# Performance work log

Measured on AMD Instinct MI355X. Metric: run time of the kernel, lower is better.

The kernel has to match this reference:

```python
import jax, jax.numpy as jnp
import numpy as np
import math

B, L, C_IN = 64, 3168, 64
D_MODEL, K = 512, 16  # K = cycle_length (kernel width == stride)
W = L // K            # 198 output tokens from deform conv


def _positional(S, d, dtype):
    # PositionalEmbedding buffer, rows [0, S)
    pos = jnp.arange(S, dtype=jnp.float32)[:, None]
    div = jnp.exp(jnp.arange(0, d, 2, dtype=jnp.float32) * (-math.log(10000.0) / d))
    pe = jnp.zeros((S, d), jnp.float32)
    pe = pe.at[:, 0::2].set(jnp.sin(pos * div))
    pe = pe.at[:, 1::2].set(jnp.cos(pos * div))
    return pe.astype(dtype)


def setup_inputs() -> dict:
    key = jax.random.key(0)
    ks = jax.random.split(key, 6)
    fan_in = C_IN * K
    std = math.sqrt(2.0 / (1 + 0.01 ** 2) / fan_in)  # kaiming_normal, leaky_relu fan_in
    return {
        "x": jax.random.normal(ks[0], (B, L, C_IN), jnp.float32),
        "w_off": jax.random.normal(ks[1], (2 * K, C_IN, K), jnp.float32) * std,
        "b_off": jax.random.normal(ks[2], (2 * K,), jnp.float32) * 0.02,
        "w_def": jax.random.normal(ks[3], (D_MODEL, C_IN, K), jnp.float32) * std,
        "b_def": jax.random.normal(ks[4], (D_MODEL,), jnp.float32) * 0.02,
        "cls_token": jax.random.normal(ks[5], (1, 1, D_MODEL), jnp.float32),
    }


def _gather_cols(xt, idx, L_):
    # xt: (B, C, L); idx: (B, K, W) int32 -> (B, C, K, W), zero out-of-bounds
    b, c = xt.shape[0], xt.shape[1]
    valid = (idx >= 0) & (idx < L_)
    idxc = jnp.clip(idx, 0, L_ - 1).reshape(b, 1, -1)
    g = jnp.take_along_axis(xt, jnp.broadcast_to(idxc, (b, c, idxc.shape[-1])), axis=2)
    g = g.reshape(b, c, idx.shape[1], idx.shape[2])
    return jnp.where(valid[:, None], g, 0.0)


def reference(x, w_off, b_off, w_def, b_def, cls_token):
    b, l, c = x.shape
    w = l // K
    # offset conv: kernel (1,K), stride (1,K) == non-overlapping windows
    xr = x[:, : w * K, :].reshape(b, w, K, c)              # (B, W, K, C)
    off = jnp.einsum('bwkc,ock->bow', xr, w_off) + b_off[None, :, None]  # (B, 2K, W)
    dy = off[:, 0::2]                                      # (B, K, W)
    dx = off[:, 1::2]
    # sampling positions along width (height is size 1, base y = 0)
    base = (jnp.arange(w)[None, :] * K + jnp.arange(K)[:, None]).astype(x.dtype)  # (K, W)
    px = base[None] + dx                                   # (B, K, W)
    x0 = jnp.floor(px)
    frac = px - x0
    x0i = x0.astype(jnp.int32)
    xt = x.transpose(0, 2, 1)                              # (B, C, L)
    v0 = _gather_cols(xt, x0i, l)
    v1 = _gather_cols(xt, x0i + 1, l)
    wy = jnp.maximum(0.0, 1.0 - jnp.abs(dy))               # vertical bilinear weight on row 0
    val = wy[:, None] * ((1.0 - frac)[:, None] * v0 + frac[:, None] * v1)  # (B, C, K, W)
    out = jnp.einsum('bckw,dck->bwd', val, w_def) + b_def  # (B, W, d_model)
    tok = jnp.concatenate([jnp.broadcast_to(cls_token, (b, 1, D_MODEL)), out], axis=1)
    pe = _positional(w + 1, D_MODEL, tok.dtype)
    return tok + pe[None]
```

## Files before the change

kernel.cpp:

```cpp
#include <hip/hip_runtime.h>
#include <math.h>
#include <stdint.h>

#define NB 64
#define NL 3168
#define NC 64
#define ND 512
#define NK 16
#define NW 198
#define NM 12672
#define KD 1024

typedef __attribute__((ext_vector_type(8))) short bf8_t;
typedef __attribute__((ext_vector_type(4))) float f4_t;

typedef const unsigned int __attribute__((address_space(1)))* as1_u32p;
typedef unsigned int __attribute__((address_space(3)))* as3_u32p;

__device__ __forceinline__ void gl_lds16(const void* g, void* l) {
  __builtin_amdgcn_global_load_lds((as1_u32p)(uintptr_t)g,
                                   (as3_u32p)(unsigned int)(uintptr_t)l, 16, 0, 0);
}

__device__ __forceinline__ unsigned short f2bf(float f) {
  union { float f; unsigned u; } v; v.f = f;
  unsigned r = v.u + 0x7FFFu + ((v.u >> 16) & 1u);
  return (unsigned short)(r >> 16);
}

__global__ void prep_kernel(const float* __restrict__ w_off, const float* __restrict__ w_def,
                            const float* __restrict__ cls, unsigned short* __restrict__ wofft,
                            unsigned short* __restrict__ wdeft, float* __restrict__ pe,
                            float* __restrict__ out) {
  int id = blockIdx.x * 256 + threadIdx.x;
  if (id < 131072) {
    float4 v = ((const float4*)w_def)[id];
    ushort4 o;
    o.x = f2bf(v.x); o.y = f2bf(v.y); o.z = f2bf(v.z); o.w = f2bf(v.w);
    ((ushort4*)wdeft)[id] = o;
    return;
  }
  id -= 131072;
  if (id < 32768) {
    int o = id >> 10, kc = id & 1023, k = kc >> 6, c = kc & 63;
    wofft[id] = f2bf(w_off[o * 1024 + c * 16 + k]);
    return;
  }
  id -= 32768;
  if (id < 101888) {
    int pos = id >> 9, d = id & 511;
    int i = d >> 1;
    float freq = expf((float)(2 * i) * (-9.210340371976184f / 512.0f));
    float arg = (float)pos * freq;
    pe[id] = (d & 1) ? cosf(arg) : sinf(arg);
    return;
  }
  id -= 101888;
  {
    int b = id >> 9, d = id & 511;
    out[(size_t)(b * 199) * 512 + d] = cls[d] + ((d & 1) ? 1.0f : 0.0f);
  }
}

__launch_bounds__(512)
__global__ void offsample_kernel(const float* __restrict__ x,
                                 const unsigned short* __restrict__ wofft,
                                 const float* __restrict__ b_off,
                                 unsigned short* __restrict__ val_ws) {
  __shared__ float partial[8][16][33];
  __shared__ float offs[16][32];
  int tid = threadIdx.x;
  int lane = tid & 63, wid = tid >> 6;
  int r16 = lane & 15, kg = lane >> 4;
  int row0 = blockIdx.x * 16;

  f4_t acc[2] = {};
  const float* arow = x + (size_t)(row0 + r16) * KD + wid * 128;
  const unsigned short* bcol0 = wofft + r16 * KD + wid * 128;
  const unsigned short* bcol1 = wofft + (16 + r16) * KD + wid * 128;

#pragma unroll
  for (int ks = 0; ks < 4; ++ks) {
    int k0 = ks * 32 + kg * 8;
    float4 v0 = *(const float4*)(arow + k0);
    float4 v1 = *(const float4*)(arow + k0 + 4);
    bf8_t a;
    a[0] = (short)f2bf(v0.x); a[1] = (short)f2bf(v0.y);
    a[2] = (short)f2bf(v0.z); a[3] = (short)f2bf(v0.w);
    a[4] = (short)f2bf(v1.x); a[5] = (short)f2bf(v1.y);
    a[6] = (short)f2bf(v1.z); a[7] = (short)f2bf(v1.w);
    bf8_t b0 = *(const bf8_t*)(bcol0 + k0);
    bf8_t b1 = *(const bf8_t*)(bcol1 + k0);
    acc[0] = __builtin_amdgcn_mfma_f32_16x16x32_bf16(a, b0, acc[0], 0, 0, 0);
    acc[1] = __builtin_amdgcn_mfma_f32_16x16x32_bf16(a, b1, acc[1], 0, 0, 0);
  }
#pragma unroll
  for (int n = 0; n < 2; ++n)
#pragma unroll
    for (int r = 0; r < 4; ++r)
      partial[wid][kg * 4 + r][n * 16 + r16] = acc[n][r];
  __syncthreads();
  {
    int r = tid >> 5, o = tid & 31;
    float s = 0.f;
#pragma unroll
    for (int w8 = 0; w8 < 8; ++w8) s += partial[w8][r][o];
    offs[r][o] = s + b_off[o];
  }
  __syncthreads();

#pragma unroll
  for (int rr = 0; rr < 2; ++rr) {
    int rp = wid * 2 + rr;
    int rg = row0 + rp;
    int b = rg / NW, w = rg - b * NW;
    const float* xb = x + (size_t)b * (NL * NC);
    unsigned short vv[16];
#pragma unroll
    for (int k = 0; k < 16; ++k) {
      float dy = offs[rp][2 * k], dx = offs[rp][2 * k + 1];
      float wy = fmaxf(0.f, 1.f - fabsf(dy));
      float px = (float)(w * 16 + k) + dx;
      float x0f = floorf(px);
      float frac = px - x0f;
      int x0 = (int)x0f;
      float v0 = (x0 >= 0 && x0 < NL) ? xb[x0 * 64 + lane] : 0.f;
      float v1 = (x0 + 1 >= 0 && x0 + 1 < NL) ? xb[(x0 + 1) * 64 + lane] : 0.f;
      vv[k] = f2bf(wy * ((1.f - frac) * v0 + frac * v1));
    }
    unsigned int p[8];
#pragma unroll
    for (int i = 0; i < 8; ++i)
      p[i] = (unsigned int)vv[2 * i] | ((unsigned int)vv[2 * i + 1] << 16);
    uint4* dst = (uint4*)(val_ws + (size_t)rg * KD + lane * 16);
    dst[0] = make_uint4(p[0], p[1], p[2], p[3]);
    dst[1] = make_uint4(p[4], p[5], p[6], p[7]);
  }
}

__launch_bounds__(384)
__global__ void gemm_kernel(const unsigned short* __restrict__ val_ws,
                            const unsigned short* __restrict__ wdeft,
                            const float* __restrict__ b_def, const float* __restrict__ pe,
                            float* __restrict__ out) {
  __shared__ unsigned short As[192 * 64];
  __shared__ unsigned short Bs[128 * 64];
  int tid = threadIdx.x;
  int flat = blockIdx.x + 4 * blockIdx.y;
  int w = (flat & 7) * 33 + (flat >> 3);
  int mt = w >> 2, nt = w & 3;
  int lane = tid & 63, wid = tid >> 6;
  int r16 = lane & 15, kg = lane >> 4;
  int wr = wid >> 1, wc = wid & 1;
  f4_t acc[4][4] = {};

  int r_st = lane >> 3;
  int j_st = lane & 7;
  const char* aBase = (const char*)val_ws + (size_t)mt * 192 * 2048;
  const char* bBase = (const char*)wdeft + (size_t)nt * 128 * 2048;
  int bsegs = (wid < 4) ? 3 : 2;
  int bbase = (wid < 4) ? wid * 3 : 12 + (wid - 4) * 2;

  for (int ks = 0; ks < 16; ++ks) {
    __syncthreads();
#pragma unroll
    for (int i = 0; i < 4; ++i) {
      int seg = wid * 4 + i;
      int r = seg * 8 + r_st;
      int src_off = ((j_st ^ (r & 7)) << 4);
      gl_lds16(aBase + (size_t)r * 2048 + ks * 128 + src_off, &As[seg * 512]);
    }
    for (int i = 0; i < bsegs; ++i) {
      int seg = bbase + i;
      int r = seg * 8 + r_st;
      int src_off = ((j_st ^ (r & 7)) << 4);
      gl_lds16(bBase + (size_t)r * 2048 + ks * 128 + src_off, &Bs[seg * 512]);
    }
    __syncthreads();
#pragma unroll
    for (int jb = 0; jb < 8; jb += 4) {
      bf8_t af[4], bf[4];
#pragma unroll
      for (int m = 0; m < 4; ++m) {
        int R = wr * 64 + m * 16 + r16;
        af[m] = *(const bf8_t*)&As[R * 64 + (((jb + kg) ^ (R & 7)) << 3)];
      }
#pragma unroll
      for (int n = 0; n < 4; ++n) {
        int Rc = wc * 64 + n * 16 + r16;
        bf[n] = *(const bf8_t*)&Bs[Rc * 64 + (((jb + kg) ^ (Rc & 7)) << 3)];
      }
#pragma unroll
      for (int m = 0; m < 4; ++m)
#pragma unroll
        for (int n = 0; n < 4; ++n)
          acc[m][n] = __builtin_amdgcn_mfma_f32_16x16x32_bf16(af[m], bf[n], acc[m][n], 0, 0, 0);
    }
  }
#pragma unroll
  for (int m = 0; m < 4; ++m)
#pragma unroll
    for (int n = 0; n < 4; ++n)
#pragma unroll
      for (int r = 0; r < 4; ++r) {
        int grow = mt * 192 + wr * 64 + m * 16 + kg * 4 + r;
        int gcol = nt * 128 + wc * 64 + n * 16 + r16;
        int bi = grow / NW, wi = grow - bi * NW;
        out[((size_t)(bi * 199 + wi + 1)) * 512 + gcol] =
            acc[m][n][r] + b_def[gcol] + pe[(wi + 1) * 512 + gcol];
      }
}

extern "C" void kernel_launch(void* const* d_in, const int* in_sizes, int n_in,
                              void* d_out, int out_size, void* d_ws, size_t ws_size,
                              hipStream_t stream) {
  const float* x     = (const float*)d_in[0];
  const float* w_off = (const float*)d_in[1];
  const float* b_off = (const float*)d_in[2];
  const float* w_def = (const float*)d_in[3];
  const float* b_def = (const float*)d_in[4];
  const float* cls   = (const float*)d_in[5];
  float* out = (float*)d_out;
  char* ws = (char*)d_ws;
  unsigned short* val_ws = (unsigned short*)ws;
  unsigned short* wofft  = (unsigned short*)(ws + 25952256);
  unsigned short* wdeft  = (unsigned short*)(ws + 26017792);
  float* pe              = (float*)(ws + 27066368);

  prep_kernel<<<1166, 256, 0, stream>>>(w_off, w_def, cls, wofft, wdeft, pe, out);
  offsample_kernel<<<NM / 16, 512, 0, stream>>>(x, wofft, b_off, val_ws);
  gemm_kernel<<<dim3(4, 66), 384, 0, stream>>>(val_ws, wdeft, b_def, pe, out);
}
```

Baseline: 67.84 us.

## Double-buffer GEMM LDS tiles and shrink tiles to 128x64 with two waves

The GEMM kernel moves from 192x128 tiles with 6 waves to 128x64 tiles with 2 waves per block, launching 792 blocks instead of 264. It double-buffers the A/B LDS stages so that loading the next K-slice overlaps compute on the current one, using explicit vmcnt waits and barriers. This aims to hide global-to-LDS latency and to fill more CUs. In exchange, B is reloaded more often because N tiles are smaller, and each block has fewer waves to cover latency.

```diff
diff --git a/kernel.cpp b/kernel.cpp
--- a/kernel.cpp
+++ b/kernel.cpp
@@ -138,57 +138,56 @@
   }
 }
 
-__launch_bounds__(384)
+__launch_bounds__(128)
 __global__ void gemm_kernel(const unsigned short* __restrict__ val_ws,
                             const unsigned short* __restrict__ wdeft,
                             const float* __restrict__ b_def, const float* __restrict__ pe,
                             float* __restrict__ out) {
-  __shared__ unsigned short As[192 * 64];
-  __shared__ unsigned short Bs[128 * 64];
+  __shared__ unsigned short As[2][128 * 64];
+  __shared__ unsigned short Bs[2][64 * 64];
   int tid = threadIdx.x;
-  int flat = blockIdx.x + 4 * blockIdx.y;
-  int w = (flat & 7) * 33 + (flat >> 3);
-  int mt = w >> 2, nt = w & 3;
+  int flat = blockIdx.x;
+  int w = (flat & 7) * 99 + (flat >> 3);
+  int mt = w >> 3, nt = w & 7;
   int lane = tid & 63, wid = tid >> 6;
   int r16 = lane & 15, kg = lane >> 4;
-  int wr = wid >> 1, wc = wid & 1;
   f4_t acc[4][4] = {};
 
   int r_st = lane >> 3;
   int j_st = lane & 7;
-  const char* aBase = (const char*)val_ws + (size_t)mt * 192 * 2048;
-  const char* bBase = (const char*)wdeft + (size_t)nt * 128 * 2048;
-  int bsegs = (wid < 4) ? 3 : 2;
-  int bbase = (wid < 4) ? wid * 3 : 12 + (wid - 4) * 2;
-
-  for (int ks = 0; ks < 16; ++ks) {
-    __syncthreads();
+  const char* aBase = (const char*)val_ws + (size_t)mt * 128 * 2048;
+  const char* bBase = (const char*)wdeft + (size_t)nt * 64 * 2048;
+
+  auto STAGE = [&](int ks, int buf) {
+#pragma unroll
+    for (int i = 0; i < 8; ++i) {
+      int seg = wid * 8 + i;
+      int r = seg * 8 + r_st;
+      int src_off = ((j_st ^ (r & 7)) << 4);
+      gl_lds16(aBase + (size_t)r * 2048 + ks * 128 + src_off, &As[buf][seg * 512]);
+    }
 #pragma unroll
     for (int i = 0; i < 4; ++i) {
       int seg = wid * 4 + i;
       int r = seg * 8 + r_st;
       int src_off = ((j_st ^ (r & 7)) << 4);
-      gl_lds16(aBase + (size_t)r * 2048 + ks * 128 + src_off, &As[seg * 512]);
-    }
-    for (int i = 0; i < bsegs; ++i) {
-      int seg = bbase + i;
-      int r = seg * 8 + r_st;
-      int src_off = ((j_st ^ (r & 7)) << 4);
-      gl_lds16(bBase + (size_t)r * 2048 + ks * 128 + src_off, &Bs[seg * 512]);
-    }
-    __syncthreads();
+      gl_lds16(bBase + (size_t)r * 2048 + ks * 128 + src_off, &Bs[buf][seg * 512]);
+    }
+  };
+
+  auto COMPUTE = [&](int buf) {
 #pragma unroll
     for (int jb = 0; jb < 8; jb += 4) {
       bf8_t af[4], bf[4];
 #pragma unroll
       for (int m = 0; m < 4; ++m) {
-        int R = wr * 64 + m * 16 + r16;
-        af[m] = *(const bf8_t*)&As[R * 64 + (((jb + kg) ^ (R & 7)) << 3)];
+        int R = wid * 64 + m * 16 + r16;
+        af[m] = *(const bf8_t*)&As[buf][R * 64 + (((jb + kg) ^ (R & 7)) << 3)];
       }
 #pragma unroll
       for (int n = 0; n < 4; ++n) {
-        int Rc = wc * 64 + n * 16 + r16;
-        bf[n] = *(const bf8_t*)&Bs[Rc * 64 + (((jb + kg) ^ (Rc & 7)) << 3)];
+        int Rc = n * 16 + r16;
+        bf[n] = *(const bf8_t*)&Bs[buf][Rc * 64 + (((jb + kg) ^ (Rc & 7)) << 3)];
       }
 #pragma unroll
       for (int m = 0; m < 4; ++m)
@@ -196,15 +195,34 @@
         for (int n = 0; n < 4; ++n)
           acc[m][n] = __builtin_amdgcn_mfma_f32_16x16x32_bf16(af[m], bf[n], acc[m][n], 0, 0, 0);
     }
-  }
+  };
+
+  STAGE(0, 0);
+  asm volatile("s_waitcnt vmcnt(0)" ::: "memory");
+  __builtin_amdgcn_s_barrier();
+#pragma unroll
+  for (int t = 0; t < 16; ++t) {
+    if (t < 15) {
+      STAGE(t + 1, (t + 1) & 1);
+      asm volatile("s_waitcnt vmcnt(12)" ::: "memory");
+    } else {
+      asm volatile("s_waitcnt vmcnt(0)" ::: "memory");
+    }
+    __builtin_amdgcn_s_barrier();
+    COMPUTE(t & 1);
+    asm volatile("s_waitcnt lgkmcnt(0)" ::: "memory");
+    __builtin_amdgcn_sched_barrier(0);
+    __builtin_amdgcn_s_barrier();
+  }
+
 #pragma unroll
   for (int m = 0; m < 4; ++m)
 #pragma unroll
     for (int n = 0; n < 4; ++n)
 #pragma unroll
       for (int r = 0; r < 4; ++r) {
-        int grow = mt * 192 + wr * 64 + m * 16 + kg * 4 + r;
-        int gcol = nt * 128 + wc * 64 + n * 16 + r16;
+        int grow = mt * 128 + wid * 64 + m * 16 + kg * 4 + r;
+        int gcol = nt * 64 + n * 16 + r16;
         int bi = grow / NW, wi = grow - bi * NW;
         out[((size_t)(bi * 199 + wi + 1)) * 512 + gcol] =
             acc[m][n][r] + b_def[gcol] + pe[(wi + 1) * 512 + gcol];
@@ -229,5 +247,5 @@
 
   prep_kernel<<<1166, 256, 0, stream>>>(w_off, w_def, cls, wofft, wdeft, pe, out);
   offsample_kernel<<<NM / 16, 512, 0, stream>>>(x, wofft, b_off, val_ws);
-  gemm_kernel<<<dim3(4, 66), 384, 0, stream>>>(val_ws, wdeft, b_def, pe, out);
-}
+  gemm_kernel<<<792, 128, 0, stream>>>(val_ws, wdeft, b_def, pe, out);
+}
```

Result: faster. 66.29 us (-2.3%).
